# Optimization experiments

Measured on AMD Instinct MI355X. Metric: run time of the kernel, lower is better.

The kernel has to match this reference:

```python
import math
import jax, jax.numpy as jnp
import numpy as np

B, S, D, H, REL_V = 2, 2048, 1024, 16, 64
HD = D // H
EPS = 1e-5


def _layernorm(x, w, b):
    # torch-style: std with Bessel correction (unbiased), divide by (std + eps)
    u = x.mean(-1, keepdims=True)
    xc = x - u
    s = jnp.sqrt((xc * xc).sum(-1, keepdims=True) / (x.shape[-1] - 1))
    return w * (xc / (s + EPS)) + b


def _gelu(x):
    return 0.5 * x * (1 + jnp.tanh(math.sqrt(2 / math.pi) * (x + 0.044715 * x ** 3)))


def setup_inputs() -> dict:
    key = jax.random.key(0)
    ks = jax.random.split(key, 6)
    wscale = 0.02
    return {
        "x": jax.random.normal(ks[0], (B, S, D), jnp.float32),
        "rel": jax.random.randint(ks[1], (B, S, S), 0, REL_V, jnp.int32),
        "ln1_w": jnp.ones((D,), jnp.float32),
        "ln1_b": jnp.zeros((D,), jnp.float32),
        "Wqkv": jax.random.normal(ks[2], (D, 3 * D), jnp.float32) * wscale,
        "bqkv": jnp.zeros((3 * D,), jnp.float32),
        "Wo": jax.random.normal(ks[3], (D, D), jnp.float32) * wscale,
        "bo": jnp.zeros((D,), jnp.float32),
        "rel_emb": jax.random.normal(ks[4], (REL_V, H), jnp.float32) * wscale,
        "ln2_w": jnp.ones((D,), jnp.float32),
        "ln2_b": jnp.zeros((D,), jnp.float32),
        "Wfc": jax.random.normal(ks[5], (D, 4 * D), jnp.float32) * wscale,
        "bfc": jnp.zeros((4 * D,), jnp.float32),
        "Wp": jax.random.normal(jax.random.fold_in(key, 7), (4 * D, D), jnp.float32) * wscale,
        "bp": jnp.zeros((D,), jnp.float32),
    }


def reference(x, rel, ln1_w, ln1_b, Wqkv, bqkv, Wo, bo, rel_emb,
              ln2_w, ln2_b, Wfc, bfc, Wp, bp):
    h = _layernorm(x, ln1_w, ln1_b)
    qkv = h @ Wqkv + bqkv  # [B,S,3D]
    q, k, v = jnp.split(qkv, 3, axis=-1)
    q = q.reshape(B, S, H, HD).transpose(0, 2, 1, 3)  # [B,H,S,HD]
    k = k.reshape(B, S, H, HD).transpose(0, 2, 1, 3)
    v = v.reshape(B, S, H, HD).transpose(0, 2, 1, 3)

    w = jnp.einsum('bhqd,bhkd->bhqk', q, k) / math.sqrt(HD)  # scale=True
    mask = jnp.tril(jnp.ones((S, S), w.dtype))  # causal tril buffer
    w = w * mask - 1e10 * (1 - mask)
    # faithful to original: rel bias multiplies masked logits (zeroing masked -1e10)
    relw = rel_emb[rel]                    # [B,S,S,H]
    relw = relw.transpose(0, 3, 1, 2)      # [B,H,S,S]
    w = w * (relw * mask)
    p = jax.nn.softmax(w, axis=-1)
    a = jnp.einsum('bhqk,bhkd->bhqd', p, v)       # [B,H,S,HD]
    a = a.transpose(0, 2, 1, 3).reshape(B, S, D)  # merge heads
    a = a @ Wo + bo

    x = x + a
    m = _gelu(_layernorm(x, ln2_w, ln2_b) @ Wfc + bfc) @ Wp + bp
    return x + m
```

## Files before the change

### kernel.cpp

```cpp
#include <hip/hip_runtime.h>
#include <hip/hip_bf16.h>
#include <math.h>

using bf16 = __hip_bfloat16;
typedef __bf16 bf16x8 __attribute__((ext_vector_type(8)));
typedef float f32x4 __attribute__((ext_vector_type(4)));

#define SEQ 2048
#define DIM 1024
#define NH 16
#define HDIM 64
#define BATCH 2

__device__ __forceinline__ void load_lds16(const bf16* g, bf16* l) {
  __builtin_amdgcn_global_load_lds((__attribute__((address_space(1))) void*)g,
                                   (__attribute__((address_space(3))) void*)l, 16, 0, 0);
}

__global__ __launch_bounds__(256) void transpose_k(const float* __restrict__ in,
                                                   bf16* __restrict__ out, int R, int C) {
  __shared__ float tile[32][33];
  int c0 = blockIdx.x * 32, r0 = blockIdx.y * 32;
  int tx = threadIdx.x, ty = threadIdx.y;
#pragma unroll
  for (int j = 0; j < 4; ++j)
    tile[ty + 8 * j][tx] = in[(size_t)(r0 + ty + 8 * j) * C + c0 + tx];
  __syncthreads();
#pragma unroll
  for (int j = 0; j < 4; ++j)
    out[(size_t)(c0 + ty + 8 * j) * R + r0 + tx] = __float2bfloat16(tile[tx][ty + 8 * j]);
}

__global__ __launch_bounds__(256) void ln_k(const float* __restrict__ x,
                                            const float* __restrict__ w,
                                            const float* __restrict__ bb,
                                            bf16* __restrict__ out) {
  int row = blockIdx.x, tid = threadIdx.x;
  int wid = tid >> 6, lane = tid & 63;
  const float* xr = x + (size_t)row * DIM;
  float v[4];
#pragma unroll
  for (int j = 0; j < 4; ++j) v[j] = xr[tid + 256 * j];
  float s = v[0] + v[1] + v[2] + v[3];
#pragma unroll
  for (int m = 1; m < 64; m <<= 1) s += __shfl_xor(s, m, 64);
  __shared__ float red[8];
  if (lane == 0) red[wid] = s;
  __syncthreads();
  float mean = (red[0] + red[1] + red[2] + red[3]) * (1.f / DIM);
  float q = 0.f;
#pragma unroll
  for (int j = 0; j < 4; ++j) {
    v[j] -= mean;
    q += v[j] * v[j];
  }
#pragma unroll
  for (int m = 1; m < 64; m <<= 1) q += __shfl_xor(q, m, 64);
  if (lane == 0) red[4 + wid] = q;
  __syncthreads();
  float ssq = red[4] + red[5] + red[6] + red[7];
  float sd = sqrtf(ssq / (float)(DIM - 1));
  float inv = 1.f / (sd + 1e-5f);
#pragma unroll
  for (int j = 0; j < 4; ++j) {
    int c = tid + 256 * j;
    float y = w[c] * (v[j] * inv) + bb[c];
    out[(size_t)row * DIM + c] = __float2bfloat16(y);
  }
}

template <int TM>
__global__ __launch_bounds__(256) void gemm_k(
    const bf16* __restrict__ A, const bf16* __restrict__ Bt, const float* __restrict__ bias,
    int M, int N, int K, int mode,
    bf16* __restrict__ o0, bf16* __restrict__ o1, bf16* __restrict__ o2,
    const float* __restrict__ residf, float* __restrict__ x2out, const float* __restrict__ x2in,
    float* __restrict__ outf) {
  constexpr int MT = TM / 32;
  constexpr int ACH = TM / 8;
  __shared__ bf16 As[TM * 64];
  __shared__ bf16 Bs[128 * 64];
  int tid = threadIdx.x;
  int wid = tid >> 6, lane = tid & 63, quad = lane >> 4, l15 = lane & 15;
  int wm = wid >> 1, wn = wid & 1;
  int m0 = blockIdx.y * TM, n0 = blockIdx.x * 128;
  int rsub = lane >> 3;
  int c8 = (lane & 7) ^ rsub;
  f32x4 acc[MT][4] = {};

  for (int k0 = 0; k0 < K; k0 += 64) {
    __syncthreads();
#pragma unroll
    for (int it = 0; it < ACH / 4; ++it) {
      int c = wid * (ACH / 4) + it;
      int row = c * 8 + rsub;
      load_lds16(A + (size_t)(m0 + row) * K + k0 + c8 * 8, &As[c * 512]);
    }
#pragma unroll
    for (int it = 0; it < 4; ++it) {
      int c = wid * 4 + it;
      int row = c * 8 + rsub;
      load_lds16(Bt + (size_t)(n0 + row) * K + k0 + c8 * 8, &Bs[c * 512]);
    }
    __syncthreads();
#pragma unroll
    for (int ks = 0; ks < 2; ++ks) {
      bf16x8 af[MT], bfr[4];
#pragma unroll
      for (int mt = 0; mt < MT; ++mt) {
        int r = wm * (MT * 16) + mt * 16 + l15;
        af[mt] = *(const bf16x8*)&As[r * 64 + ((ks * 4 + quad) ^ (r & 7)) * 8];
      }
#pragma unroll
      for (int nt = 0; nt < 4; ++nt) {
        int r = wn * 64 + nt * 16 + l15;
        bfr[nt] = *(const bf16x8*)&Bs[r * 64 + ((ks * 4 + quad) ^ (r & 7)) * 8];
      }
#pragma unroll
      for (int mt = 0; mt < MT; ++mt)
#pragma unroll
        for (int nt = 0; nt < 4; ++nt)
          acc[mt][nt] =
              __builtin_amdgcn_mfma_f32_16x16x32_bf16(af[mt], bfr[nt], acc[mt][nt], 0, 0, 0);
    }
  }

#pragma unroll
  for (int mt = 0; mt < MT; ++mt) {
#pragma unroll
    for (int nt = 0; nt < 4; ++nt) {
      int col = n0 + wn * 64 + nt * 16 + l15;
      float bv = bias[col];
      int row_base = m0 + wm * (MT * 16) + mt * 16 + quad * 4;
      if (mode == 0) {
        int which = col >> 10, d = col & 1023, hh = d >> 6, dd = d & 63;
        int b = row_base >> 11, s2 = row_base & 2047;
        if (which == 2) {
          unsigned short pk[4];
#pragma unroll
          for (int r = 0; r < 4; ++r)
            pk[r] = __bfloat16_as_ushort(__float2bfloat16(acc[mt][nt][r] + bv));
          *(uint2*)&o2[(((size_t)b * NH + hh) * HDIM + dd) * SEQ + s2] = *(uint2*)pk;
        } else {
          bf16* dst = which == 0 ? o0 : o1;
#pragma unroll
          for (int r = 0; r < 4; ++r)
            dst[(((size_t)b * NH + hh) * SEQ + s2 + r) * HDIM + dd] =
                __float2bfloat16(acc[mt][nt][r] + bv);
        }
      } else {
#pragma unroll
        for (int r = 0; r < 4; ++r) {
          int row = row_base + r;
          float val = acc[mt][nt][r] + bv;
          if (mode == 1) {
            size_t i = (size_t)row * N + col;
            x2out[i] = residf[i] + val;
          } else if (mode == 2) {
            float t = val;
            float u = 0.7978845608028654f * (t + 0.044715f * t * t * t);
            float g = t / (1.f + __expf(-2.f * u));
            o0[(size_t)row * N + col] = __float2bfloat16(g);
          } else {
            size_t i = (size_t)row * N + col;
            outf[i] = x2in[i] + val;
          }
        }
      }
    }
  }
}

__global__ __launch_bounds__(256) void sufv_k(const bf16* __restrict__ vt,
                                              float* __restrict__ suf) {
  int row = blockIdx.x;
  const bf16* src = vt + (size_t)row * SEQ;
  float* dst = suf + (size_t)row * SEQ;
  int tid = threadIdx.x;
  float v[8];
  float s = 0.f;
#pragma unroll
  for (int j = 0; j < 8; ++j) {
    v[j] = __bfloat162float(src[tid * 8 + j]);
    s += v[j];
  }
  __shared__ float sc[256];
  sc[tid] = s;
  __syncthreads();
  for (int off = 1; off < 256; off <<= 1) {
    float add = (tid + off < 256) ? sc[tid + off] : 0.f;
    __syncthreads();
    sc[tid] += add;
    __syncthreads();
  }
  float run = (tid < 255) ? sc[tid + 1] : 0.f;
#pragma unroll
  for (int j = 7; j >= 0; --j) {
    dst[tid * 8 + j] = run;
    run += v[j];
  }
}

__device__ __forceinline__ int pswz(int row) { return (row & 7) ^ (((row >> 3) & 1) << 1); }

__global__ __launch_bounds__(256) void attn_k(const bf16* __restrict__ q,
                                              const bf16* __restrict__ k,
                                              const bf16* __restrict__ v,
                                              const int* __restrict__ rel,
                                              const float* __restrict__ rel_emb,
                                              const float* __restrict__ suf,
                                              bf16* __restrict__ out) {
  int h = blockIdx.x;
  int qt = (SEQ / 64 - 1) - blockIdx.y;
  int b = blockIdx.z;
  int tid = threadIdx.x;
  int wid = tid >> 6, lane = tid & 63, quad = lane >> 4, l15 = lane & 15;

  __shared__ __align__(16) char SM[40960];
  bf16* Kb = (bf16*)SM;
  bf16* Vb = (bf16*)(SM + 16384);
  bf16* Ps = (bf16*)(SM + 32768);
  float(*SufLds)[68] = (float(*)[68])SM;

  const size_t bh = (size_t)b * NH + h;
  const bf16* qb = q + (bh * SEQ + (size_t)qt * 64) * HDIM;
  const bf16* kb0 = k + bh * SEQ * HDIM;
  const bf16* vt0 = v + bh * (size_t)HDIM * SEQ;

  float rv = 0.125f * rel_emb[lane * NH + h];

  int rsub = lane >> 3;
  int c8 = (lane & 7) ^ rsub;

  bf16x8 aq[2];
#pragma unroll
  for (int ks = 0; ks < 2; ++ks)
    aq[ks] = *(const bf16x8*)(qb + (size_t)(wid * 16 + l15) * HDIM + ks * 32 + quad * 8);

#pragma unroll
  for (int it = 0; it < 2; ++it) {
    int c = wid * 2 + it;
    int row = c * 8 + rsub;
    load_lds16(kb0 + (size_t)row * HDIM + c8 * 8, &Kb[c * 512]);
    load_lds16(vt0 + (size_t)row * SEQ + c8 * 8, &Vb[c * 512]);
  }

  const int* relq = rel + (size_t)b * SEQ * SEQ + (size_t)qt * 64 * SEQ;
  const int* rp[4];
#pragma unroll
  for (int r = 0; r < 4; ++r) rp[r] = relq + (size_t)(wid * 16 + quad * 4 + r) * SEQ;

  int ridx[4][4];
#pragma unroll
  for (int nt = 0; nt < 4; ++nt)
#pragma unroll
    for (int r = 0; r < 4; ++r) ridx[nt][r] = rp[r][nt * 16 + l15];

  __syncthreads();

  const int q_base = qt * 64 + wid * 16 + quad * 4;
  const int prow_w = wid * 16 + quad * 4;
  const int prow_r = wid * 16 + l15;
  const int psw_r = pswz(prow_r);
  float l_part[4] = {0.f, 0.f, 0.f, 0.f};
  f32x4 o_acc[4] = {};

  for (int kt = 0; kt < qt; ++kt) {
    int cur = kt & 1;

    int ridx2[4][4];
    {
      bf16* Kd = Kb + (cur ^ 1) * 4096;
      bf16* Vd = Vb + (cur ^ 1) * 4096;
#pragma unroll
      for (int it = 0; it < 2; ++it) {
        int c = wid * 2 + it;
        int row = c * 8 + rsub;
        load_lds16(kb0 + (size_t)((kt + 1) * 64 + row) * HDIM + c8 * 8, &Kd[c * 512]);
        load_lds16(vt0 + (size_t)row * SEQ + (kt + 1) * 64 + c8 * 8, &Vd[c * 512]);
      }
#pragma unroll
      for (int nt = 0; nt < 4; ++nt)
#pragma unroll
        for (int r = 0; r < 4; ++r) ridx2[nt][r] = rp[r][(kt + 1) * 64 + nt * 16 + l15];
    }

    const bf16* Ksb = Kb + cur * 4096;
    const bf16* Vtb = Vb + cur * 4096;

    f32x4 sacc[4] = {};
    __builtin_amdgcn_s_setprio(1);
#pragma unroll
    for (int ks = 0; ks < 2; ++ks) {
#pragma unroll
      for (int nt = 0; nt < 4; ++nt) {
        bf16x8 bfr = *(const bf16x8*)&Ksb[(nt * 16 + l15) * 64 + ((ks * 4 + quad) ^ (l15 & 7)) * 8];
        sacc[nt] = __builtin_amdgcn_mfma_f32_16x16x32_bf16(aq[ks], bfr, sacc[nt], 0, 0, 0);
      }
    }
    __builtin_amdgcn_s_setprio(0);

#pragma unroll
    for (int nt = 0; nt < 4; ++nt) {
#pragma unroll
      for (int r = 0; r < 4; ++r) {
        float m = __shfl(rv, ridx[nt][r], 64);
        float p = __expf(sacc[nt][r] * m);
        l_part[r] += p;
        int row = prow_w + r;
        int sw = (nt * 2 + (l15 >> 3)) ^ pswz(row);
        Ps[row * 64 + sw * 8 + (l15 & 7)] = __float2bfloat16(p);
      }
    }

    __builtin_amdgcn_s_setprio(1);
#pragma unroll
    for (int ks = 0; ks < 2; ++ks) {
      bf16x8 af = *(const bf16x8*)&Ps[prow_r * 64 + ((ks * 4 + quad) ^ psw_r) * 8];
#pragma unroll
      for (int nt = 0; nt < 4; ++nt) {
        bf16x8 bfr = *(const bf16x8*)&Vtb[(nt * 16 + l15) * 64 + ((ks * 4 + quad) ^ (l15 & 7)) * 8];
        o_acc[nt] = __builtin_amdgcn_mfma_f32_16x16x32_bf16(af, bfr, o_acc[nt], 0, 0, 0);
      }
    }
    __builtin_amdgcn_s_setprio(0);

    __syncthreads();

#pragma unroll
    for (int nt = 0; nt < 4; ++nt)
#pragma unroll
      for (int r = 0; r < 4; ++r) ridx[nt][r] = ridx2[nt][r];
  }

  {
    int cur = qt & 1;
    const bf16* Ksb = Kb + cur * 4096;
    const bf16* Vtb = Vb + cur * 4096;

    f32x4 sacc[4] = {};
    __builtin_amdgcn_s_setprio(1);
#pragma unroll
    for (int ks = 0; ks < 2; ++ks) {
#pragma unroll
      for (int nt = 0; nt < 4; ++nt) {
        bf16x8 bfr = *(const bf16x8*)&Ksb[(nt * 16 + l15) * 64 + ((ks * 4 + quad) ^ (l15 & 7)) * 8];
        sacc[nt] = __builtin_amdgcn_mfma_f32_16x16x32_bf16(aq[ks], bfr, sacc[nt], 0, 0, 0);
      }
    }
    __builtin_amdgcn_s_setprio(0);

#pragma unroll
    for (int nt = 0; nt < 4; ++nt) {
#pragma unroll
      for (int r = 0; r < 4; ++r) {
        float m = __shfl(rv, ridx[nt][r], 64);
        float p = __expf(sacc[nt][r] * m);
        int k_abs = qt * 64 + nt * 16 + l15;
        if (k_abs > q_base + r) p = 0.f;
        l_part[r] += p;
        int row = prow_w + r;
        int sw = (nt * 2 + (l15 >> 3)) ^ pswz(row);
        Ps[row * 64 + sw * 8 + (l15 & 7)] = __float2bfloat16(p);
      }
    }

    __builtin_amdgcn_s_setprio(1);
#pragma unroll
    for (int ks = 0; ks < 2; ++ks) {
      bf16x8 af = *(const bf16x8*)&Ps[prow_r * 64 + ((ks * 4 + quad) ^ psw_r) * 8];
#pragma unroll
      for (int nt = 0; nt < 4; ++nt) {
        bf16x8 bfr = *(const bf16x8*)&Vtb[(nt * 16 + l15) * 64 + ((ks * 4 + quad) ^ (l15 & 7)) * 8];
        o_acc[nt] = __builtin_amdgcn_mfma_f32_16x16x32_bf16(af, bfr, o_acc[nt], 0, 0, 0);
      }
    }
    __builtin_amdgcn_s_setprio(0);

    __syncthreads();
  }

#pragma unroll
  for (int r = 0; r < 4; ++r)
#pragma unroll
    for (int m = 1; m < 16; m <<= 1) l_part[r] += __shfl_xor(l_part[r], m, 64);

  const float* sufb = suf + bh * (size_t)HDIM * SEQ + (size_t)qt * 64;
#pragma unroll
  for (int p = 0; p < 4; ++p) {
    int idx = p * 256 + tid;
    int d = idx >> 4, qq = idx & 15;
    *(float4*)&SufLds[d][qq * 4] = *(const float4*)(sufb + (size_t)d * SEQ + qq * 4);
  }
  __syncthreads();

#pragma unroll
  for (int nt = 0; nt < 4; ++nt) {
    int d = nt * 16 + l15;
#pragma unroll
    for (int r = 0; r < 4; ++r) {
      int row = q_base + r;
      int cnt = (SEQ - 1) - row;
      float l = l_part[r] + (float)cnt;
      int q_local = wid * 16 + quad * 4 + r;
      float ov = (o_acc[nt][r] + SufLds[d][q_local]) / l;
      out[((size_t)b * SEQ + row) * DIM + h * HDIM + d] = __float2bfloat16(ov);
    }
  }
}

extern "C" void kernel_launch(void* const* d_in, const int* in_sizes, int n_in,
                              void* d_out, int out_size, void* d_ws, size_t ws_size,
                              hipStream_t stream) {
  const float* x = (const float*)d_in[0];
  const int* rel = (const int*)d_in[1];
  const float* ln1w = (const float*)d_in[2];
  const float* ln1b = (const float*)d_in[3];
  const float* Wqkv = (const float*)d_in[4];
  const float* bqkv = (const float*)d_in[5];
  const float* Wo = (const float*)d_in[6];
  const float* bo = (const float*)d_in[7];
  const float* rel_emb = (const float*)d_in[8];
  const float* ln2w = (const float*)d_in[9];
  const float* ln2b = (const float*)d_in[10];
  const float* Wfc = (const float*)d_in[11];
  const float* bfc = (const float*)d_in[12];
  const float* Wp = (const float*)d_in[13];
  const float* bp = (const float*)d_in[14];
  float* outp = (float*)d_out;

  char* ws = (char*)d_ws;
  const size_t MB = 1u << 20;
  bf16* h = (bf16*)(ws + 0);
  bf16* qb = (bf16*)(ws + 8 * MB);
  bf16* kb = (bf16*)(ws + 16 * MB);
  bf16* vb = (bf16*)(ws + 24 * MB);
  float* x2 = (float*)(ws + 32 * MB);
  float* suf = (float*)(ws + 32 * MB);
  bf16* fcb = (bf16*)(ws + 48 * MB);
  bf16* wqkvT = (bf16*)(ws + 48 * MB);
  bf16* woT = (bf16*)(ws + 54 * MB);
  bf16* wfcT = (bf16*)(ws + 16 * MB);
  bf16* wpT = (bf16*)(ws + 24 * MB);

  dim3 tb(32, 8);
  transpose_k<<<dim3(3072 / 32, 1024 / 32), tb, 0, stream>>>(Wqkv, wqkvT, 1024, 3072);
  transpose_k<<<dim3(1024 / 32, 1024 / 32), tb, 0, stream>>>(Wo, woT, 1024, 1024);

  ln_k<<<BATCH * SEQ, 256, 0, stream>>>(x, ln1w, ln1b, h);

  gemm_k<128><<<dim3(3072 / 128, 4096 / 128), 256, 0, stream>>>(
      h, wqkvT, bqkv, BATCH * SEQ, 3072, 1024, 0, qb, kb, vb, nullptr, nullptr, nullptr,
      nullptr);

  sufv_k<<<BATCH * NH * HDIM, 256, 0, stream>>>(vb, suf);

  attn_k<<<dim3(NH, SEQ / 64, BATCH), 256, 0, stream>>>(qb, kb, vb, rel, rel_emb, suf, h);

  gemm_k<64><<<dim3(1024 / 128, 4096 / 64), 256, 0, stream>>>(
      h, woT, bo, BATCH * SEQ, 1024, 1024, 1, nullptr, nullptr, nullptr, x, x2, nullptr,
      nullptr);

  transpose_k<<<dim3(4096 / 32, 1024 / 32), tb, 0, stream>>>(Wfc, wfcT, 1024, 4096);
  transpose_k<<<dim3(1024 / 32, 4096 / 32), tb, 0, stream>>>(Wp, wpT, 4096, 1024);

  ln_k<<<BATCH * SEQ, 256, 0, stream>>>(x2, ln2w, ln2b, qb);

  gemm_k<128><<<dim3(4096 / 128, 4096 / 128), 256, 0, stream>>>(
      qb, wfcT, bfc, BATCH * SEQ, 4096, 1024, 2, fcb, nullptr, nullptr, nullptr, nullptr,
      nullptr, nullptr);

  gemm_k<64><<<dim3(1024 / 128, 4096 / 64), 256, 0, stream>>>(
      fcb, wpT, bp, BATCH * SEQ, 1024, 4096, 3, nullptr, nullptr, nullptr, nullptr, nullptr, x2,
      outp);
}
```

Before: 424.0 us.

## Double-buffer GEMM LDS tiles with async prefetch and swizzle workgroup order

Converts the GEMM main loop to a two-stage LDS ring: tiles for step t+2 are issued via global_load_lds while step t is computed, using partial vmcnt waits instead of full syncs. It also remaps the block index with an 8-way swizzle for better L2 locality and raises wave priority around the MFMA block. This doubles LDS usage, which can lower occupancy. The hardcoded vmcnt counts must match the number of loads issued per stage.

```diff
diff --git a/kernel.cpp b/kernel.cpp
--- a/kernel.cpp
+++ b/kernel.cpp
@@ -78,51 +78,78 @@
     float* __restrict__ outf) {
   constexpr int MT = TM / 32;
   constexpr int ACH = TM / 8;
-  __shared__ bf16 As[TM * 64];
-  __shared__ bf16 Bs[128 * 64];
+  __shared__ bf16 As[2][TM * 64];
+  __shared__ bf16 Bs[2][128 * 64];
   int tid = threadIdx.x;
   int wid = tid >> 6, lane = tid & 63, quad = lane >> 4, l15 = lane & 15;
   int wm = wid >> 1, wn = wid & 1;
-  int m0 = blockIdx.y * TM, n0 = blockIdx.x * 128;
+  int nwg = gridDim.x * gridDim.y;
+  int flat = blockIdx.y * gridDim.x + blockIdx.x;
+  int swz = (flat & 7) * (nwg >> 3) + (flat >> 3);
+  int m0 = (swz / gridDim.x) * TM, n0 = (swz % gridDim.x) * 128;
   int rsub = lane >> 3;
   int c8 = (lane & 7) ^ rsub;
   f32x4 acc[MT][4] = {};
-
-  for (int k0 = 0; k0 < K; k0 += 64) {
-    __syncthreads();
+  const int nt = K >> 6;
+
+  auto stage = [&](int t, int buf) {
+    int k0 = t * 64;
 #pragma unroll
     for (int it = 0; it < ACH / 4; ++it) {
       int c = wid * (ACH / 4) + it;
       int row = c * 8 + rsub;
-      load_lds16(A + (size_t)(m0 + row) * K + k0 + c8 * 8, &As[c * 512]);
+      load_lds16(A + (size_t)(m0 + row) * K + k0 + c8 * 8, &As[buf][c * 512]);
     }
 #pragma unroll
     for (int it = 0; it < 4; ++it) {
       int c = wid * 4 + it;
       int row = c * 8 + rsub;
-      load_lds16(Bt + (size_t)(n0 + row) * K + k0 + c8 * 8, &Bs[c * 512]);
-    }
-    __syncthreads();
+      load_lds16(Bt + (size_t)(n0 + row) * K + k0 + c8 * 8, &Bs[buf][c * 512]);
+    }
+  };
+
+  stage(0, 0);
+  stage(1, 1);
+
+  for (int t = 0; t < nt; ++t) {
+    int cur = t & 1;
+    if (t + 1 < nt) {
+      if constexpr (TM == 128) asm volatile("s_waitcnt vmcnt(8)" ::: "memory");
+      else                     asm volatile("s_waitcnt vmcnt(6)" ::: "memory");
+    } else {
+      asm volatile("s_waitcnt vmcnt(0)" ::: "memory");
+    }
+    __builtin_amdgcn_sched_barrier(0);
+    __builtin_amdgcn_s_barrier();
+    __builtin_amdgcn_sched_barrier(0);
+    const bf16* Ac = As[cur];
+    const bf16* Bc = Bs[cur];
 #pragma unroll
     for (int ks = 0; ks < 2; ++ks) {
       bf16x8 af[MT], bfr[4];
 #pragma unroll
       for (int mt = 0; mt < MT; ++mt) {
         int r = wm * (MT * 16) + mt * 16 + l15;
-        af[mt] = *(const bf16x8*)&As[r * 64 + ((ks * 4 + quad) ^ (r & 7)) * 8];
-      }
-#pragma unroll
-      for (int nt = 0; nt < 4; ++nt) {
-        int r = wn * 64 + nt * 16 + l15;
-        bfr[nt] = *(const bf16x8*)&Bs[r * 64 + ((ks * 4 + quad) ^ (r & 7)) * 8];
-      }
+        af[mt] = *(const bf16x8*)&Ac[r * 64 + ((ks * 4 + quad) ^ (r & 7)) * 8];
+      }
+#pragma unroll
+      for (int nt2 = 0; nt2 < 4; ++nt2) {
+        int r = wn * 64 + nt2 * 16 + l15;
+        bfr[nt2] = *(const bf16x8*)&Bc[r * 64 + ((ks * 4 + quad) ^ (r & 7)) * 8];
+      }
+      __builtin_amdgcn_s_setprio(1);
 #pragma unroll
       for (int mt = 0; mt < MT; ++mt)
 #pragma unroll
-        for (int nt = 0; nt < 4; ++nt)
-          acc[mt][nt] =
-              __builtin_amdgcn_mfma_f32_16x16x32_bf16(af[mt], bfr[nt], acc[mt][nt], 0, 0, 0);
-    }
+        for (int nt2 = 0; nt2 < 4; ++nt2)
+          acc[mt][nt2] =
+              __builtin_amdgcn_mfma_f32_16x16x32_bf16(af[mt], bfr[nt2], acc[mt][nt2], 0, 0, 0);
+      __builtin_amdgcn_s_setprio(0);
+    }
+    __builtin_amdgcn_sched_barrier(0);
+    __builtin_amdgcn_s_barrier();
+    __builtin_amdgcn_sched_barrier(0);
+    if (t + 2 < nt) stage(t + 2, cur);
   }
 
 #pragma unroll
@@ -157,9 +184,9 @@
             size_t i = (size_t)row * N + col;
             x2out[i] = residf[i] + val;
           } else if (mode == 2) {
-            float t = val;
-            float u = 0.7978845608028654f * (t + 0.044715f * t * t * t);
-            float g = t / (1.f + __expf(-2.f * u));
+            float t2 = val;
+            float u = 0.7978845608028654f * (t2 + 0.044715f * t2 * t2 * t2);
+            float g = t2 / (1.f + __expf(-2.f * u));
             o0[(size_t)row * N + col] = __float2bfloat16(g);
           } else {
             size_t i = (size_t)row * N + col;
```

New measurement: 433.1 us. +2.1%, slower.

## Add 256x256-tile pipelined GEMM kernel for QKV and FC projections

Applied to the files above, without the earlier changes.

Introduces a 512-thread GEMM with 256x256 output tiles, a double-buffered 128KB LDS layout split into half-K stages, explicit vmcnt waits and barriers, and MFMA priority raising. It replaces the 128x128-tile kernel for the QKV and FC GEMMs to raise arithmetic intensity and overlap global loads with MFMA work. The older kernel is reduced to the residual-add epilogues. The large tiles shrink the grid (192 blocks for QKV), which may underfill the CUs, and the heavy LDS use limits occupancy to one block per CU.

```diff
diff --git a/kernel.cpp b/kernel.cpp
--- a/kernel.cpp
+++ b/kernel.cpp
@@ -69,11 +69,135 @@
   }
 }
 
+__global__ __launch_bounds__(512) void gemm256_k(
+    const bf16* __restrict__ A, const bf16* __restrict__ Bt, const float* __restrict__ bias,
+    int N, int K, int mode, bf16* __restrict__ o0, bf16* __restrict__ o1,
+    bf16* __restrict__ o2) {
+  __shared__ bf16 LDSb[65536];
+  int tid = threadIdx.x;
+  int wid = tid >> 6, lane = tid & 63, quad = lane >> 4, l15 = lane & 15;
+  int wm = wid >> 2, wn = wid & 3;
+  int m0 = blockIdx.y * 256, n0 = blockIdx.x * 256;
+  int grow = lane >> 2;
+  int gslot = (lane & 3) ^ ((lane >> 3) & 3);
+  const int nt = K >> 6;
+
+  float bv[4];
+#pragma unroll
+  for (int nf = 0; nf < 4; ++nf) bv[nf] = bias[n0 + wn * 64 + nf * 16 + l15];
+
+  auto stageA = [&](int tile, int ks) {
+    int bd = tile & 1;
+#pragma unroll
+    for (int it = 0; it < 2; ++it) {
+      int c = wid * 2 + it;
+      load_lds16(A + (size_t)(m0 + c * 16 + grow) * K + tile * 64 + ks * 32 + gslot * 8,
+                 &LDSb[bd * 32768 + ks * 8192 + c * 512]);
+    }
+  };
+  auto stageB = [&](int tile, int ks) {
+    int bd = tile & 1;
+#pragma unroll
+    for (int it = 0; it < 2; ++it) {
+      int c = wid * 2 + it;
+      load_lds16(Bt + (size_t)(n0 + c * 16 + grow) * K + tile * 64 + ks * 32 + gslot * 8,
+                 &LDSb[bd * 32768 + 16384 + ks * 8192 + c * 512]);
+    }
+  };
+
+  f32x4 acc[8][4] = {};
+
+  stageA(0, 0); stageB(0, 0);
+  stageA(0, 1); stageB(0, 1);
+  stageA(1, 0); stageB(1, 0);
+  asm volatile("s_waitcnt vmcnt(8)" ::: "memory");
+  __builtin_amdgcn_sched_barrier(0);
+  __builtin_amdgcn_s_barrier();
+  __builtin_amdgcn_sched_barrier(0);
+
+#define PHASE(BD, KS, MH, STAGE_STMT, WAIT_STMT)                                             \
+  {                                                                                          \
+    bf16x8 af[4], bq[4];                                                                     \
+    _Pragma("unroll") for (int j = 0; j < 4; ++j) {                                          \
+      int r = wm * 128 + (MH) * 64 + j * 16 + l15;                                           \
+      af[j] = *(const bf16x8*)&LDSb[(BD) * 32768 + (KS) * 8192 + (r >> 4) * 512 +            \
+                                    (r & 15) * 32 + ((quad ^ ((r >> 1) & 3)) << 3)];         \
+    }                                                                                        \
+    _Pragma("unroll") for (int n = 0; n < 4; ++n) {                                          \
+      int r = wn * 64 + n * 16 + l15;                                                        \
+      bq[n] = *(const bf16x8*)&LDSb[(BD) * 32768 + 16384 + (KS) * 8192 + (r >> 4) * 512 +    \
+                                    (r & 15) * 32 + ((quad ^ ((r >> 1) & 3)) << 3)];         \
+    }                                                                                        \
+    STAGE_STMT;                                                                              \
+    __builtin_amdgcn_sched_barrier(0);                                                       \
+    __builtin_amdgcn_s_barrier();                                                            \
+    __builtin_amdgcn_sched_barrier(0);                                                       \
+    __builtin_amdgcn_s_setprio(1);                                                           \
+    _Pragma("unroll") for (int j = 0; j < 4; ++j)                                            \
+        _Pragma("unroll") for (int n = 0; n < 4; ++n)                                        \
+            acc[(MH) * 4 + j][n] = __builtin_amdgcn_mfma_f32_16x16x32_bf16(                  \
+                af[j], bq[n], acc[(MH) * 4 + j][n], 0, 0, 0);                                \
+    __builtin_amdgcn_s_setprio(0);                                                           \
+    WAIT_STMT;                                                                               \
+    __builtin_amdgcn_sched_barrier(0);                                                       \
+    __builtin_amdgcn_s_barrier();                                                            \
+    __builtin_amdgcn_sched_barrier(0);                                                       \
+  }
+
+  for (int t = 0; t < nt; ++t) {
+    int bd = t & 1;
+    PHASE(bd, 0, 0, { if (t + 1 < nt) stageA(t + 1, 1); }, {});
+    PHASE(bd, 0, 1, { if (t + 1 < nt) stageB(t + 1, 1); }, {
+      if (t + 1 < nt) asm volatile("s_waitcnt vmcnt(8)" ::: "memory");
+      else            asm volatile("s_waitcnt vmcnt(0)" ::: "memory");
+    });
+    PHASE(bd, 1, 0, { if (t + 2 < nt) stageA(t + 2, 0); }, {});
+    PHASE(bd, 1, 1, { if (t + 2 < nt) stageB(t + 2, 0); }, {
+      if (t + 2 < nt)      asm volatile("s_waitcnt vmcnt(8)" ::: "memory");
+      else if (t + 1 < nt) asm volatile("s_waitcnt vmcnt(4)" ::: "memory");
+    });
+  }
+#undef PHASE
+
+#pragma unroll
+  for (int mf = 0; mf < 8; ++mf) {
+#pragma unroll
+    for (int nf = 0; nf < 4; ++nf) {
+      int col = n0 + wn * 64 + nf * 16 + l15;
+      int row_base = m0 + wm * 128 + mf * 16 + quad * 4;
+      if (mode == 0) {
+        int which = col >> 10, d = col & 1023, hh = d >> 6, dd = d & 63;
+        int b = row_base >> 11, s2 = row_base & 2047;
+        if (which == 2) {
+          unsigned short pk[4];
+#pragma unroll
+          for (int r = 0; r < 4; ++r)
+            pk[r] = __bfloat16_as_ushort(__float2bfloat16(acc[mf][nf][r] + bv[nf]));
+          *(uint2*)&o2[(((size_t)b * NH + hh) * HDIM + dd) * SEQ + s2] = *(uint2*)pk;
+        } else {
+          bf16* dst = which == 0 ? o0 : o1;
+#pragma unroll
+          for (int r = 0; r < 4; ++r)
+            dst[(((size_t)b * NH + hh) * SEQ + s2 + r) * HDIM + dd] =
+                __float2bfloat16(acc[mf][nf][r] + bv[nf]);
+        }
+      } else {
+#pragma unroll
+        for (int r = 0; r < 4; ++r) {
+          float t2 = acc[mf][nf][r] + bv[nf];
+          float u = 0.7978845608028654f * (t2 + 0.044715f * t2 * t2 * t2);
+          float g = t2 / (1.f + __expf(-2.f * u));
+          o0[(size_t)(row_base + r) * N + col] = __float2bfloat16(g);
+        }
+      }
+    }
+  }
+}
+
 template <int TM>
 __global__ __launch_bounds__(256) void gemm_k(
     const bf16* __restrict__ A, const bf16* __restrict__ Bt, const float* __restrict__ bias,
     int M, int N, int K, int mode,
-    bf16* __restrict__ o0, bf16* __restrict__ o1, bf16* __restrict__ o2,
     const float* __restrict__ residf, float* __restrict__ x2out, const float* __restrict__ x2in,
     float* __restrict__ outf) {
   constexpr int MT = TM / 32;
@@ -112,16 +236,16 @@
         af[mt] = *(const bf16x8*)&As[r * 64 + ((ks * 4 + quad) ^ (r & 7)) * 8];
       }
 #pragma unroll
-      for (int nt = 0; nt < 4; ++nt) {
-        int r = wn * 64 + nt * 16 + l15;
-        bfr[nt] = *(const bf16x8*)&Bs[r * 64 + ((ks * 4 + quad) ^ (r & 7)) * 8];
+      for (int nt2 = 0; nt2 < 4; ++nt2) {
+        int r = wn * 64 + nt2 * 16 + l15;
+        bfr[nt2] = *(const bf16x8*)&Bs[r * 64 + ((ks * 4 + quad) ^ (r & 7)) * 8];
       }
 #pragma unroll
       for (int mt = 0; mt < MT; ++mt)
 #pragma unroll
-        for (int nt = 0; nt < 4; ++nt)
-          acc[mt][nt] =
-              __builtin_amdgcn_mfma_f32_16x16x32_bf16(af[mt], bfr[nt], acc[mt][nt], 0, 0, 0);
+        for (int nt2 = 0; nt2 < 4; ++nt2)
+          acc[mt][nt2] =
+              __builtin_amdgcn_mfma_f32_16x16x32_bf16(af[mt], bfr[nt2], acc[mt][nt2], 0, 0, 0);
     }
   }
 
@@ -130,42 +254,15 @@
 #pragma unroll
     for (int nt = 0; nt < 4; ++nt) {
       int col = n0 + wn * 64 + nt * 16 + l15;
-      float bv = bias[col];
+      float bvs = bias[col];
       int row_base = m0 + wm * (MT * 16) + mt * 16 + quad * 4;
-      if (mode == 0) {
-        int which = col >> 10, d = col & 1023, hh = d >> 6, dd = d & 63;
-        int b = row_base >> 11, s2 = row_base & 2047;
-        if (which == 2) {
-          unsigned short pk[4];
-#pragma unroll
-          for (int r = 0; r < 4; ++r)
-            pk[r] = __bfloat16_as_ushort(__float2bfloat16(acc[mt][nt][r] + bv));
-          *(uint2*)&o2[(((size_t)b * NH + hh) * HDIM + dd) * SEQ + s2] = *(uint2*)pk;
-        } else {
-          bf16* dst = which == 0 ? o0 : o1;
-#pragma unroll
-          for (int r = 0; r < 4; ++r)
-            dst[(((size_t)b * NH + hh) * SEQ + s2 + r) * HDIM + dd] =
-                __float2bfloat16(acc[mt][nt][r] + bv);
-        }
-      } else {
-#pragma unroll
-        for (int r = 0; r < 4; ++r) {
-          int row = row_base + r;
-          float val = acc[mt][nt][r] + bv;
-          if (mode == 1) {
-            size_t i = (size_t)row * N + col;
-            x2out[i] = residf[i] + val;
-          } else if (mode == 2) {
-            float t = val;
-            float u = 0.7978845608028654f * (t + 0.044715f * t * t * t);
-            float g = t / (1.f + __expf(-2.f * u));
-            o0[(size_t)row * N + col] = __float2bfloat16(g);
-          } else {
-            size_t i = (size_t)row * N + col;
-            outf[i] = x2in[i] + val;
-          }
-        }
+#pragma unroll
+      for (int r = 0; r < 4; ++r) {
+        int row = row_base + r;
+        float val = acc[mt][nt][r] + bvs;
+        size_t i = (size_t)row * N + col;
+        if (mode == 1) x2out[i] = residf[i] + val;
+        else           outf[i] = x2in[i] + val;
       }
     }
   }
@@ -267,7 +364,6 @@
 
   for (int kt = 0; kt < qt; ++kt) {
     int cur = kt & 1;
-
     int ridx2[4][4];
     {
       bf16* Kd = Kb + (cur ^ 1) * 4096;
@@ -449,28 +545,24 @@
 
   ln_k<<<BATCH * SEQ, 256, 0, stream>>>(x, ln1w, ln1b, h);
 
-  gemm_k<128><<<dim3(3072 / 128, 4096 / 128), 256, 0, stream>>>(
-      h, wqkvT, bqkv, BATCH * SEQ, 3072, 1024, 0, qb, kb, vb, nullptr, nullptr, nullptr,
-      nullptr);
+  gemm256_k<<<dim3(3072 / 256, 4096 / 256), 512, 0, stream>>>(
+      h, wqkvT, bqkv, 3072, 1024, 0, qb, kb, vb);
 
   sufv_k<<<BATCH * NH * HDIM, 256, 0, stream>>>(vb, suf);
 
   attn_k<<<dim3(NH, SEQ / 64, BATCH), 256, 0, stream>>>(qb, kb, vb, rel, rel_emb, suf, h);
 
   gemm_k<64><<<dim3(1024 / 128, 4096 / 64), 256, 0, stream>>>(
-      h, woT, bo, BATCH * SEQ, 1024, 1024, 1, nullptr, nullptr, nullptr, x, x2, nullptr,
-      nullptr);
+      h, woT, bo, BATCH * SEQ, 1024, 1024, 1, x, x2, nullptr, nullptr);
 
   transpose_k<<<dim3(4096 / 32, 1024 / 32), tb, 0, stream>>>(Wfc, wfcT, 1024, 4096);
   transpose_k<<<dim3(1024 / 32, 4096 / 32), tb, 0, stream>>>(Wp, wpT, 4096, 1024);
 
   ln_k<<<BATCH * SEQ, 256, 0, stream>>>(x2, ln2w, ln2b, qb);
 
-  gemm_k<128><<<dim3(4096 / 128, 4096 / 128), 256, 0, stream>>>(
-      qb, wfcT, bfc, BATCH * SEQ, 4096, 1024, 2, fcb, nullptr, nullptr, nullptr, nullptr,
-      nullptr, nullptr);
+  gemm256_k<<<dim3(4096 / 256, 4096 / 256), 512, 0, stream>>>(
+      qb, wfcT, bfc, 4096, 1024, 2, fcb, nullptr, nullptr);
 
   gemm_k<64><<<dim3(1024 / 128, 4096 / 64), 256, 0, stream>>>(
-      fcb, wpT, bp, BATCH * SEQ, 1024, 4096, 3, nullptr, nullptr, nullptr, nullptr, nullptr, x2,
-      outp);
-}
+      fcb, wpT, bp, BATCH * SEQ, 1024, 4096, 3, nullptr, nullptr, x2, outp);
+}
```

New measurement: 404.5 us. 1.05x faster.
